# Optimization experiments

Hardware: AMD Instinct MI355X
Metric: run time of the kernel (lower is better)

Reference implementation:

```python
import jax, jax.numpy as jnp
import numpy as np

N = 50000          # nodes
E = 1_600_000      # edges
DIN = 128          # input feature dim
HID = 32           # hidden_dim per head
HEADS = 4          # conv1 heads
G = 64             # graphs in batch
SLOPE = 0.2        # LeakyReLU negative slope (PyG GATConv default)
EPS = 1e-16


def setup_inputs() -> dict:
    key = jax.random.key(0)
    ks = jax.random.split(key, 14)
    s = 0.05
    return {
        "x": jax.random.normal(ks[0], (N, DIN), jnp.float32),
        "edge_index": jax.random.randint(ks[1], (2, E), 0, N, dtype=jnp.int64),
        "batch": jnp.sort(jax.random.randint(ks[2], (N,), 0, G, dtype=jnp.int64)),
        # conv1: GATConv(DIN, HID, heads=4, concat=True)
        "W1": jax.random.normal(ks[3], (DIN, HEADS * HID), jnp.float32) * s,
        "a_src1": jax.random.normal(ks[4], (HEADS, HID), jnp.float32) * s,
        "a_dst1": jax.random.normal(ks[5], (HEADS, HID), jnp.float32) * s,
        "b1": jax.random.normal(ks[6], (HEADS * HID,), jnp.float32) * s,
        # conv2: GATConv(4*HID, HID, heads=1)
        "W2": jax.random.normal(ks[7], (HEADS * HID, HID), jnp.float32) * s,
        "a_src2": jax.random.normal(ks[8], (1, HID), jnp.float32) * s,
        "a_dst2": jax.random.normal(ks[9], (1, HID), jnp.float32) * s,
        "b2": jax.random.normal(ks[10], (HID,), jnp.float32) * s,
        # final Linear(HID, 2)
        "Wfc": jax.random.normal(ks[11], (HID, 2), jnp.float32) * s,
        "bfc": jax.random.normal(ks[12], (2,), jnp.float32) * s,
    }


def gat_conv(x, src, dst, W, a_src, a_dst, b, heads, d):
    """PyG-style GATConv (self-loops already appended to src/dst)."""
    n = x.shape[0]
    h = (x @ W).reshape(n, heads, d)                   # [N,H,D]
    alpha_src = jnp.einsum('nhd,hd->nh', h, a_src)     # [N,H]
    alpha_dst = jnp.einsum('nhd,hd->nh', h, a_dst)     # [N,H]
    e = alpha_src[src] + alpha_dst[dst]                # [Etot,H]
    e = jnp.where(e >= 0, e, SLOPE * e)                # LeakyReLU
    # segment softmax over destination nodes
    m = jax.ops.segment_max(e, dst, num_segments=n)    # [N,H]
    e = jnp.exp(e - m[dst])
    s = jax.ops.segment_sum(e, dst, num_segments=n)    # [N,H]
    alpha = e / (s[dst] + EPS)                         # [Etot,H]
    msg = h[src] * alpha[:, :, None]                   # [Etot,H,D]
    out = jax.ops.segment_sum(msg, dst, num_segments=n)  # [N,H,D]
    return out.reshape(n, heads * d) + b               # concat heads + bias


def reference(x, edge_index, batch, W1, a_src1, a_dst1, b1,
              W2, a_src2, a_dst2, b2, Wfc, bfc):
    n = x.shape[0]
    loops = jnp.arange(n, dtype=edge_index.dtype)
    src = jnp.concatenate([edge_index[0], loops])      # add self loops
    dst = jnp.concatenate([edge_index[1], loops])

    h = gat_conv(x, src, dst, W1, a_src1, a_dst1, b1, HEADS, HID)
    h = jax.nn.elu(h)
    h = gat_conv(h, src, dst, W2, a_src2, a_dst2, b2, 1, HID)
    h = jax.nn.elu(h)

    # global mean pool over graphs
    sums = jax.ops.segment_sum(h, batch, num_segments=G)            # [G,HID]
    cnt = jax.ops.segment_sum(jnp.ones((n, 1), h.dtype), batch, num_segments=G)
    pooled = sums / jnp.maximum(cnt, 1.0)

    logits = pooled @ Wfc + bfc                                      # [G,2]
    return jax.nn.log_softmax(logits, axis=1)
```

## Files before the change

### kernel.cpp

```cpp
#include <hip/hip_runtime.h>
#include <hip/hip_fp8.h>
#include <math.h>

#define DIN   128
#define HEADS 4
#define HID   32
#define C1    (HEADS*HID)
#define NG    64
#define SLOPE 0.2f
#define EPSF  1e-16f

#define NPB   256
#define CAPQ  10240
#define CHUNK 2048

__device__ __forceinline__ unsigned int f2bf(float f) {
    unsigned int u = __float_as_uint(f);
    return (u + 0x7FFFu + ((u >> 16) & 1u)) >> 16;
}
__device__ __forceinline__ float bf_lo(unsigned int u) { return __uint_as_float(u << 16); }
__device__ __forceinline__ float bf_hi(unsigned int u) { return __uint_as_float(u & 0xFFFF0000u); }

__device__ __forceinline__ unsigned int f2fp8(float f) {
    __hip_fp8_e4m3 t(f);
    return (unsigned int)t.__x;
}
template <int SEL>
__device__ __forceinline__ float fp8tof(unsigned int u) {
#if __has_builtin(__builtin_amdgcn_cvt_f32_fp8)
    return __builtin_amdgcn_cvt_f32_fp8(u, SEL);
#else
    __hip_fp8_e4m3 t; t.__x = (unsigned char)((u >> (8 * SEL)) & 0xFFu); return (float)t;
#endif
}

template <int NT>
__device__ __forceinline__ int blockScanExcl(int v, int* wsum) {
    int lane = threadIdx.x & 63, wid = threadIdx.x >> 6;
    int incl = v;
#pragma unroll
    for (int d = 1; d < 64; d <<= 1) {
        int t = __shfl_up(incl, d);
        if (lane >= d) incl += t;
    }
    if (lane == 63) wsum[wid] = incl;
    __syncthreads();
    if (threadIdx.x == 0) {
        int a = 0;
#pragma unroll
        for (int w = 0; w < NT / 64; w++) { int t = wsum[w]; wsum[w] = a; a += t; }
    }
    __syncthreads();
    return incl - v + wsum[wid];
}

__global__ void k_zero(int* gcursor, float* pooled, int nbuck) {
    int i = blockIdx.x * blockDim.x + threadIdx.x;
    if (i < nbuck) gcursor[i] = 0;
    if (i < NG * HID) pooled[i] = 0.0f;
}

__global__ __launch_bounds__(256) void k_binscatter(const int* __restrict__ srcs,
        const int* __restrict__ dsts, int* __restrict__ gcursor,
        unsigned int* __restrict__ stage, int E) {
    __shared__ unsigned int s_tmp[CHUNK];
    __shared__ unsigned int s_out[CHUNK];
    __shared__ int s_hist[256], s_off[256], s_base[256], s_cur[256], wsum[4];
    int tid = threadIdx.x;
    int e0 = blockIdx.x * CHUNK;
    int cnt = min(CHUNK, E - e0);
    s_hist[tid] = 0;
    __syncthreads();
    for (int i = tid; i < cnt; i += 256) {
        int sv = srcs[e0 + i];
        int dv = dsts[e0 + i];
        int b = dv >> 8;
        s_tmp[i] = ((unsigned)b << 24) | ((unsigned)(dv & (NPB - 1)) << 16) | (unsigned)sv;
        atomicAdd(&s_hist[b], 1);
    }
    __syncthreads();
    int myc = s_hist[tid];
    int excl = blockScanExcl<256>(myc, wsum);
    s_off[tid] = excl;
    s_base[tid] = myc ? atomicAdd(&gcursor[tid], myc) : 0;
    s_cur[tid] = 0;
    __syncthreads();
    for (int i = tid; i < cnt; i += 256) {
        unsigned int p = s_tmp[i];
        int b = p >> 24;
        int pos = s_off[b] + atomicAdd(&s_cur[b], 1);
        s_out[pos] = p;
    }
    __syncthreads();
    for (int i = tid; i < cnt; i += 256) {
        unsigned int p = s_out[i];
        int b = p >> 24;
        int rel = s_base[b] + (i - s_off[b]);
        if (rel < CAPQ) stage[(size_t)b * CAPQ + rel] = p & 0xFFFFFFu;
    }
}

__global__ void k_bucketscan(int* __restrict__ gcursor, int* __restrict__ ebase, int nbuck) {
    __shared__ int wsum[4];
    int tid = threadIdx.x;
    int c = (tid < nbuck) ? min(gcursor[tid], CAPQ) : 0;
    int excl = blockScanExcl<256>(c, wsum);
    if (tid < nbuck) { ebase[tid] = excl; gcursor[tid] = c; }
}

__global__ __launch_bounds__(512) void k_bucket_build(const unsigned int* __restrict__ stage,
        const int* __restrict__ gcursor, const int* __restrict__ ebase,
        int* __restrict__ rowstart, int* __restrict__ rowlen,
        int* __restrict__ esrc, int n) {
    __shared__ unsigned int s_e[CAPQ];
    __shared__ int s_cnt[256], s_offn[256], s_curn[256], wsum[8];
    int bx = blockIdx.x, tid = threadIdx.x;
    int b = bx >> 1, hf = bx & 1;
    int cnt = gcursor[b];
    int eb = ebase[b];
    int node0 = b << 8;
    for (int i = tid; i < cnt; i += 512) s_e[i] = stage[(size_t)b * CAPQ + i];
    if (tid < 256) { s_cnt[tid] = 0; s_curn[tid] = 0; }
    __syncthreads();
    for (int i = tid; i < cnt; i += 512) atomicAdd(&s_cnt[s_e[i] >> 16], 1);
    __syncthreads();
    int myc = (tid < 256) ? s_cnt[tid] : 0;
    int excl = blockScanExcl<512>(myc, wsum);
    if (tid < 256) s_offn[tid] = excl;
    __syncthreads();
    if (tid < 128) {
        int ld = (hf << 7) + tid;
        int node = node0 + ld;
        if (node < n) { rowstart[node] = eb + s_offn[ld]; rowlen[node] = s_cnt[ld]; }
    }
    for (int i = tid; i < cnt; i += 512) {
        unsigned int p = s_e[i];
        int ld = p >> 16;
        if ((ld >> 7) == hf) {
            int pos = s_offn[ld] + atomicAdd(&s_curn[ld], 1);
            esrc[eb + pos] = (int)(p & 0xFFFFu);
        }
    }
}

#define BM1 64
#define BK1 32
__global__ __launch_bounds__(256) void k_conv1(const float* __restrict__ x, const float* __restrict__ W1,
                        const float* __restrict__ a_src, const float* __restrict__ a_dst,
                        unsigned char* __restrict__ h1f8, float* __restrict__ as1,
                        float* __restrict__ ad1, int n) {
    __shared__ float xt[BK1][BM1 + 1];
    __shared__ float ws[BK1][C1];
    int tid = threadIdx.x;
    int m0 = blockIdx.x * BM1;
    int ty = tid >> 4;
    int tx = tid & 15;
    int r0 = ty * 4;
    int c0 = tx * 8;
    float acc[4][8];
#pragma unroll
    for (int i = 0; i < 4; i++)
#pragma unroll
        for (int j = 0; j < 8; j++) acc[i][j] = 0.0f;

    for (int kb = 0; kb < DIN; kb += BK1) {
        {
            int row = tid >> 3;
            int c4  = (tid & 7) * 4;
#pragma unroll
            for (int i = 0; i < 2; i++) {
                int rr = row + i * 32;
                int g = m0 + rr;
                float4 v = make_float4(0.f, 0.f, 0.f, 0.f);
                if (g < n) v = *reinterpret_cast<const float4*>(x + (size_t)g * DIN + kb + c4);
                xt[c4 + 0][rr] = v.x; xt[c4 + 1][rr] = v.y;
                xt[c4 + 2][rr] = v.z; xt[c4 + 3][rr] = v.w;
            }
            int c4w = (tid & 31) * 4;
            int k0  = tid >> 5;
#pragma unroll
            for (int i = 0; i < 4; i++) {
                int kk = k0 + i * 8;
                *reinterpret_cast<float4*>(&ws[kk][c4w]) =
                    *reinterpret_cast<const float4*>(W1 + (size_t)(kb + kk) * C1 + c4w);
            }
        }
        __syncthreads();
#pragma unroll
        for (int kk = 0; kk < BK1; kk++) {
            float a[4], bb[8];
            *reinterpret_cast<float4*>(a)      = *reinterpret_cast<float4*>(&xt[kk][r0]);
            *reinterpret_cast<float4*>(bb)     = *reinterpret_cast<float4*>(&ws[kk][c0]);
            *reinterpret_cast<float4*>(bb + 4) = *reinterpret_cast<float4*>(&ws[kk][c0 + 4]);
#pragma unroll
            for (int i = 0; i < 4; i++)
#pragma unroll
                for (int j = 0; j < 8; j++) acc[i][j] = fmaf(a[i], bb[j], acc[i][j]);
        }
        __syncthreads();
    }
    float asv[8], adv[8];
#pragma unroll
    for (int j = 0; j < 8; j++) { asv[j] = a_src[c0 + j]; adv[j] = a_dst[c0 + j]; }
#pragma unroll
    for (int i = 0; i < 4; i++) {
        int g = m0 + r0 + i;
        float ps = 0.0f, pd = 0.0f;
#pragma unroll
        for (int j = 0; j < 8; j++) {
            ps = fmaf(acc[i][j], asv[j], ps);
            pd = fmaf(acc[i][j], adv[j], pd);
        }
        if (g < n) {
            unsigned int w0 = 0, w1 = 0;
#pragma unroll
            for (int j = 0; j < 4; j++) w0 |= f2fp8(acc[i][j]) << (8 * j);
#pragma unroll
            for (int j = 0; j < 4; j++) w1 |= f2fp8(acc[i][4 + j]) << (8 * j);
            *reinterpret_cast<uint2*>(h1f8 + (size_t)g * C1 + c0) = make_uint2(w0, w1);
        }
        ps += __shfl_xor(ps, 1); ps += __shfl_xor(ps, 2);
        pd += __shfl_xor(pd, 1); pd += __shfl_xor(pd, 2);
        if ((tx & 3) == 0 && g < n) {
            as1[g * HEADS + (tx >> 2)] = ps;
            ad1[g * HEADS + (tx >> 2)] = pd;
        }
    }
}

#define BM2 128
#define BK2 32
__global__ __launch_bounds__(256) void k_conv2(const unsigned int* __restrict__ x2u,
                        const float* __restrict__ W2,
                        const float* __restrict__ a_src, const float* __restrict__ a_dst,
                        unsigned char* __restrict__ h2f8, float* __restrict__ as2,
                        float* __restrict__ ad2, int n) {
    __shared__ float xt[BK2][BM2 + 1];
    __shared__ float ws[BK2][HID];
    int tid = threadIdx.x;
    int m0 = blockIdx.x * BM2;
    int ty = tid >> 3;
    int tx = tid & 7;
    int r0 = ty * 4;
    int c0 = tx * 4;
    float acc[4][4];
#pragma unroll
    for (int i = 0; i < 4; i++)
#pragma unroll
        for (int j = 0; j < 4; j++) acc[i][j] = 0.0f;

    for (int kb = 0; kb < C1; kb += BK2) {
        {
            int row = tid >> 3;
            int c4  = (tid & 7) * 4;
#pragma unroll
            for (int i = 0; i < 4; i++) {
                int rr = row + i * 32;
                int g = m0 + rr;
                uint2 u = make_uint2(0u, 0u);
                if (g < n) u = *reinterpret_cast<const uint2*>(x2u + (size_t)g * 64 + ((kb + c4) >> 1));
                xt[c4 + 0][rr] = bf_lo(u.x); xt[c4 + 1][rr] = bf_hi(u.x);
                xt[c4 + 2][rr] = bf_lo(u.y); xt[c4 + 3][rr] = bf_hi(u.y);
            }
            int kk = tid >> 3;
            int c4w = (tid & 7) * 4;
            *reinterpret_cast<float4*>(&ws[kk][c4w]) =
                *reinterpret_cast<const float4*>(W2 + (size_t)(kb + kk) * HID + c4w);
        }
        __syncthreads();
#pragma unroll
        for (int kk = 0; kk < BK2; kk++) {
            float a[4], bb[4];
            *reinterpret_cast<float4*>(a)  = *reinterpret_cast<float4*>(&xt[kk][r0]);
            *reinterpret_cast<float4*>(bb) = *reinterpret_cast<float4*>(&ws[kk][c0]);
#pragma unroll
            for (int i = 0; i < 4; i++)
#pragma unroll
                for (int j = 0; j < 4; j++) acc[i][j] = fmaf(a[i], bb[j], acc[i][j]);
        }
        __syncthreads();
    }
    float asv[4], adv[4];
#pragma unroll
    for (int j = 0; j < 4; j++) { asv[j] = a_src[c0 + j]; adv[j] = a_dst[c0 + j]; }
#pragma unroll
    for (int i = 0; i < 4; i++) {
        int g = m0 + r0 + i;
        float ps = 0.0f, pd = 0.0f;
#pragma unroll
        for (int j = 0; j < 4; j++) {
            ps = fmaf(acc[i][j], asv[j], ps);
            pd = fmaf(acc[i][j], adv[j], pd);
        }
        if (g < n) {
            unsigned int w = 0;
#pragma unroll
            for (int j = 0; j < 4; j++) w |= f2fp8(acc[i][j]) << (8 * j);
            *reinterpret_cast<unsigned int*>(h2f8 + (size_t)g * HID + c0) = w;
        }
        ps += __shfl_xor(ps, 1); ps += __shfl_xor(ps, 2); ps += __shfl_xor(ps, 4);
        pd += __shfl_xor(pd, 1); pd += __shfl_xor(pd, 2); pd += __shfl_xor(pd, 4);
        if (tx == 0 && g < n) { as2[g] = ps; ad2[g] = pd; }
    }
}

__global__ __launch_bounds__(256) void k_gat1(const int* __restrict__ rowstart, const int* __restrict__ rowlen,
                       const int* __restrict__ esrc,
                       const float* __restrict__ as1, const float* __restrict__ ad1,
                       const unsigned char* __restrict__ h1f8, const float* __restrict__ b1,
                       unsigned int* __restrict__ x2u, int n) {
    __shared__ float alds[4][64 * HEADS];
    __shared__ int   slds[4][64];
    const unsigned short* h1h = (const unsigned short*)h1f8;
    int wid = threadIdx.x >> 6;
    int lane = threadIdx.x & 63;
    int nid = blockIdx.x * 4 + wid;
    bool active = nid < n;
    int start = 0, deg = 0, cnt = 1;
    if (active) { start = rowstart[nid]; deg = rowlen[nid]; cnt = deg + 1; }
    bool fast = active && (cnt <= 64);

    float adv[HEADS] = {0.f, 0.f, 0.f, 0.f};
    if (active) {
#pragma unroll
        for (int h = 0; h < HEADS; h++) adv[h] = ad1[nid * HEADS + h];
    }

    if (fast) {
        int s = nid;
        if (lane < deg) s = esrc[start + lane];
        bool act = lane < cnt;
        float4 asv = make_float4(0.f, 0.f, 0.f, 0.f);
        if (act) asv = *reinterpret_cast<const float4*>(as1 + (size_t)s * HEADS);
        float v[HEADS];
        v[0] = asv.x + adv[0]; v[1] = asv.y + adv[1];
        v[2] = asv.z + adv[2]; v[3] = asv.w + adv[3];
        float p[HEADS], sum[HEADS];
#pragma unroll
        for (int h = 0; h < HEADS; h++) {
            v[h] = (v[h] >= 0.0f) ? v[h] : SLOPE * v[h];
            p[h] = act ? __expf(v[h]) : 0.0f;
            sum[h] = p[h];
#pragma unroll
            for (int off = 32; off; off >>= 1) sum[h] += __shfl_xor(sum[h], off);
            p[h] *= 1.0f / (sum[h] + EPSF);
        }
        slds[wid][lane] = s;
        float4 pv; pv.x = p[0]; pv.y = p[1]; pv.z = p[2]; pv.w = p[3];
        *reinterpret_cast<float4*>(&alds[wid][lane * 4]) = pv;
    }
    __syncthreads();
    if (!active) return;

    int j = lane * 2;
    int hme = lane >> 4;
    if (fast) {
        float accx = 0.0f, accy = 0.0f;
        int k = 0;
        for (; k + 3 < cnt; k += 4) {
            int s0 = slds[wid][k],     s1 = slds[wid][k + 1];
            int s2 = slds[wid][k + 2], s3 = slds[wid][k + 3];
            float a0 = alds[wid][k * 4 + hme],       a1 = alds[wid][(k + 1) * 4 + hme];
            float a2 = alds[wid][(k + 2) * 4 + hme], a3 = alds[wid][(k + 3) * 4 + hme];
            unsigned int u0 = h1h[(size_t)s0 * 64 + lane];
            unsigned int u1 = h1h[(size_t)s1 * 64 + lane];
            unsigned int u2 = h1h[(size_t)s2 * 64 + lane];
            unsigned int u3 = h1h[(size_t)s3 * 64 + lane];
            accx = fmaf(fp8tof<0>(u0), a0, accx); accy = fmaf(fp8tof<1>(u0), a0, accy);
            accx = fmaf(fp8tof<0>(u1), a1, accx); accy = fmaf(fp8tof<1>(u1), a1, accy);
            accx = fmaf(fp8tof<0>(u2), a2, accx); accy = fmaf(fp8tof<1>(u2), a2, accy);
            accx = fmaf(fp8tof<0>(u3), a3, accx); accy = fmaf(fp8tof<1>(u3), a3, accy);
        }
        for (; k < cnt; k++) {
            int s0 = slds[wid][k];
            float a0 = alds[wid][k * 4 + hme];
            unsigned int u0 = h1h[(size_t)s0 * 64 + lane];
            accx = fmaf(fp8tof<0>(u0), a0, accx); accy = fmaf(fp8tof<1>(u0), a0, accy);
        }
        float o0 = accx + b1[j], o1 = accy + b1[j + 1];
        o0 = (o0 > 0.0f) ? o0 : expm1f(o0);
        o1 = (o1 > 0.0f) ? o1 : expm1f(o1);
        x2u[(size_t)nid * 64 + lane] = f2bf(o0) | (f2bf(o1) << 16);
    } else {
        float m[HEADS] = {-INFINITY, -INFINITY, -INFINITY, -INFINITY};
        for (int k = lane; k <= deg; k += 64) {
            int s = (k < deg) ? esrc[start + k] : nid;
#pragma unroll
            for (int h = 0; h < HEADS; h++) {
                float v = as1[s * HEADS + h] + adv[h];
                v = (v >= 0.0f) ? v : SLOPE * v;
                m[h] = fmaxf(m[h], v);
            }
        }
#pragma unroll
        for (int h = 0; h < HEADS; h++)
#pragma unroll
            for (int off = 32; off; off >>= 1) m[h] = fmaxf(m[h], __shfl_xor(m[h], off));
        float sum[HEADS] = {0.f, 0.f, 0.f, 0.f};
        for (int k = lane; k <= deg; k += 64) {
            int s = (k < deg) ? esrc[start + k] : nid;
#pragma unroll
            for (int h = 0; h < HEADS; h++) {
                float v = as1[s * HEADS + h] + adv[h];
                v = (v >= 0.0f) ? v : SLOPE * v;
                sum[h] += __expf(v - m[h]);
            }
        }
#pragma unroll
        for (int h = 0; h < HEADS; h++) {
#pragma unroll
            for (int off = 32; off; off >>= 1) sum[h] += __shfl_xor(sum[h], off);
            sum[h] = 1.0f / (sum[h] + EPSF);
        }
        float adme = adv[hme], mme = m[hme], invme = sum[hme];
        float accx = 0.0f, accy = 0.0f;
        for (int k = 0; k <= deg; k++) {
            int s = (k < deg) ? esrc[start + k] : nid;
            float v = as1[s * HEADS + hme] + adme;
            v = (v >= 0.0f) ? v : SLOPE * v;
            float alpha = __expf(v - mme) * invme;
            unsigned int u0 = h1h[(size_t)s * 64 + lane];
            accx = fmaf(fp8tof<0>(u0), alpha, accx);
            accy = fmaf(fp8tof<1>(u0), alpha, accy);
        }
        float o0 = accx + b1[j], o1 = accy + b1[j + 1];
        o0 = (o0 > 0.0f) ? o0 : expm1f(o0);
        o1 = (o1 > 0.0f) ? o1 : expm1f(o1);
        x2u[(size_t)nid * 64 + lane] = f2bf(o0) | (f2bf(o1) << 16);
    }
}

__global__ __launch_bounds__(256) void k_gat2(const int* __restrict__ rowstart, const int* __restrict__ rowlen,
                       const int* __restrict__ esrc,
                       const float* __restrict__ as2, const float* __restrict__ ad2,
                       const unsigned char* __restrict__ h2f8, const float* __restrict__ b2,
                       float* __restrict__ x3, int n) {
    __shared__ float alds[4][64];
    __shared__ int   slds[4][64];
    const unsigned short* h2h = (const unsigned short*)h2f8;
    int wid = threadIdx.x >> 6;
    int lane = threadIdx.x & 63;
    int nid = blockIdx.x * 4 + wid;
    bool active = nid < n;
    int start = 0, deg = 0, cnt = 1;
    float adv = 0.0f;
    if (active) { start = rowstart[nid]; deg = rowlen[nid]; cnt = deg + 1; adv = ad2[nid]; }
    bool fast = active && (cnt <= 64);

    if (fast) {
        int s = nid;
        if (lane < deg) s = esrc[start + lane];
        bool act = lane < cnt;
        float v = as2[s] + adv;
        v = (v >= 0.0f) ? v : SLOPE * v;
        float p = act ? __expf(v) : 0.0f;
        float sum = p;
#pragma unroll
        for (int off = 32; off; off >>= 1) sum += __shfl_xor(sum, off);
        p *= 1.0f / (sum + EPSF);
        slds[wid][lane] = s;
        alds[wid][lane] = p;
    }
    __syncthreads();
    if (!active) return;

    if (fast) {
        int q = lane >> 4, l = lane & 15;
        float acc0 = 0.0f, acc1 = 0.0f;
#pragma unroll 2
        for (int k = q; k < cnt; k += 4) {
            int s = slds[wid][k];
            float a = alds[wid][k];
            unsigned int u = h2h[(size_t)s * 16 + l];
            acc0 = fmaf(fp8tof<0>(u), a, acc0);
            acc1 = fmaf(fp8tof<1>(u), a, acc1);
        }
        acc0 += __shfl_xor(acc0, 16); acc0 += __shfl_xor(acc0, 32);
        acc1 += __shfl_xor(acc1, 16); acc1 += __shfl_xor(acc1, 32);
        if (q == 0) {
            int c0 = l * 2;
            float o0 = acc0 + b2[c0], o1 = acc1 + b2[c0 + 1];
            o0 = (o0 > 0.0f) ? o0 : expm1f(o0);
            o1 = (o1 > 0.0f) ? o1 : expm1f(o1);
            float2 r; r.x = o0; r.y = o1;
            *reinterpret_cast<float2*>(x3 + (size_t)nid * HID + c0) = r;
        }
    } else {
        int c = lane & 31;
        int half = lane >> 5;
        float m = -INFINITY;
        for (int k = lane; k <= deg; k += 64) {
            int s = (k < deg) ? esrc[start + k] : nid;
            float v = as2[s] + adv;
            v = (v >= 0.0f) ? v : SLOPE * v;
            m = fmaxf(m, v);
        }
#pragma unroll
        for (int off = 32; off; off >>= 1) m = fmaxf(m, __shfl_xor(m, off));
        float sum = 0.0f;
        for (int k = lane; k <= deg; k += 64) {
            int s = (k < deg) ? esrc[start + k] : nid;
            float v = as2[s] + adv;
            v = (v >= 0.0f) ? v : SLOPE * v;
            sum += __expf(v - m);
        }
#pragma unroll
        for (int off = 32; off; off >>= 1) sum += __shfl_xor(sum, off);
        float inv = 1.0f / (sum + EPSF);
        float acc = 0.0f;
        for (int k = half; k <= deg; k += 2) {
            int s = (k < deg) ? esrc[start + k] : nid;
            float v = as2[s] + adv;
            v = (v >= 0.0f) ? v : SLOPE * v;
            float alpha = __expf(v - m) * inv;
            unsigned int u = h2h[(size_t)s * 16 + (c >> 1)];
            float hv = (c & 1) ? fp8tof<1>(u) : fp8tof<0>(u);
            acc = fmaf(hv, alpha, acc);
        }
        acc += __shfl_xor(acc, 32);
        if (half == 0) {
            float o = acc + b2[c];
            o = (o > 0.0f) ? o : expm1f(o);
            x3[(size_t)nid * HID + c] = o;
        }
    }
}

__device__ __forceinline__ int lower_bound_g(const int* batch, int n, int g) {
    int lo = 0, hi = n;
    while (lo < hi) {
        int mid = (lo + hi) >> 1;
        if (batch[mid] < g) lo = mid + 1; else hi = mid;
    }
    return lo;
}

__global__ void k_pool(const float* __restrict__ x3, const int* __restrict__ batch,
                       float* __restrict__ pooled, int n) {
    int g = blockIdx.x >> 2, part = blockIdx.x & 3;
    int start = lower_bound_g(batch, n, g);
    int end   = lower_bound_g(batch, n, g + 1);
    int c = threadIdx.x & 31;
    int row = threadIdx.x >> 5;
    float acc = 0.0f;
    for (int i = start + part * 8 + row; i < end; i += 32)
        acc += x3[(size_t)i * HID + c];
    __shared__ float sacc[8][HID];
    sacc[row][c] = acc;
    __syncthreads();
    if (row == 0) {
        float a = 0.0f;
#pragma unroll
        for (int p = 0; p < 8; p++) a += sacc[p][c];
        atomicAdd(&pooled[g * HID + c], a);
    }
}

__global__ void k_head(const float* __restrict__ pooled, const int* __restrict__ batch, int n,
                       const float* __restrict__ Wfc, const float* __restrict__ bfc,
                       float* __restrict__ out, int g_count) {
    int g = blockIdx.x * blockDim.x + threadIdx.x;
    if (g >= g_count) return;
    int start = lower_bound_g(batch, n, g);
    int end   = lower_bound_g(batch, n, g + 1);
    float inv = 1.0f / fmaxf((float)(end - start), 1.0f);
    float l0 = bfc[0], l1 = bfc[1];
#pragma unroll
    for (int d = 0; d < HID; d++) {
        float p = pooled[g * HID + d] * inv;
        l0 = fmaf(p, Wfc[d * 2 + 0], l0);
        l1 = fmaf(p, Wfc[d * 2 + 1], l1);
    }
    float mx = fmaxf(l0, l1);
    float lse = mx + logf(expf(l0 - mx) + expf(l1 - mx));
    out[g * 2 + 0] = l0 - lse;
    out[g * 2 + 1] = l1 - lse;
}

extern "C" void kernel_launch(void* const* d_in, const int* in_sizes, int n_in,
                              void* d_out, int out_size, void* d_ws, size_t ws_size,
                              hipStream_t stream) {
    const float* x      = (const float*)d_in[0];
    const int*   ei     = (const int*)d_in[1];
    const int*   batch  = (const int*)d_in[2];
    const float* W1     = (const float*)d_in[3];
    const float* a_src1 = (const float*)d_in[4];
    const float* a_dst1 = (const float*)d_in[5];
    const float* b1     = (const float*)d_in[6];
    const float* W2     = (const float*)d_in[7];
    const float* a_src2 = (const float*)d_in[8];
    const float* a_dst2 = (const float*)d_in[9];
    const float* b2     = (const float*)d_in[10];
    const float* Wfc    = (const float*)d_in[11];
    const float* bfc    = (const float*)d_in[12];
    float* out = (float*)d_out;

    const int n = in_sizes[2];
    const int E = in_sizes[1] / 2;
    const int nbuck = (n + NPB - 1) / NPB;

    const int* srcs = ei;
    const int* dsts = ei + E;

    unsigned char* h1f8 = (unsigned char*)d_ws;
    unsigned int*  x2u  = (unsigned int*)(h1f8 + (size_t)n * C1);
    unsigned char* h2f8 = (unsigned char*)(x2u + (size_t)n * 64);
    float* x3     = (float*)(h2f8 + (size_t)n * HID);
    float* as1    = x3  + (size_t)n * HID;
    float* ad1    = as1 + (size_t)n * HEADS;
    float* as2    = ad1 + (size_t)n * HEADS;
    float* ad2    = as2 + (size_t)n;
    float* pooled = ad2 + (size_t)n;
    int* rowstart = (int*)(pooled + NG * HID);
    int* rowlen   = rowstart + n;
    int* esrc     = rowlen + n;
    int* gcursor  = esrc + E;
    int* ebase    = gcursor + 256;
    unsigned int* stage = (unsigned int*)(ebase + 256);

    k_zero<<<8, 256, 0, stream>>>(gcursor, pooled, nbuck);
    k_binscatter<<<(E + CHUNK - 1) / CHUNK, 256, 0, stream>>>(srcs, dsts, gcursor, stage, E);
    k_bucketscan<<<1, 256, 0, stream>>>(gcursor, ebase, nbuck);
    k_bucket_build<<<nbuck * 2, 512, 0, stream>>>(stage, gcursor, ebase, rowstart, rowlen, esrc, n);

    k_conv1<<<(n + BM1 - 1) / BM1, 256, 0, stream>>>(x, W1, a_src1, a_dst1, h1f8, as1, ad1, n);

    k_gat1<<<(n + 3) / 4, 256, 0, stream>>>(rowstart, rowlen, esrc, as1, ad1, h1f8, b1, x2u, n);

    k_conv2<<<(n + BM2 - 1) / BM2, 256, 0, stream>>>(x2u, W2, a_src2, a_dst2, h2f8, as2, ad2, n);

    k_gat2<<<(n + 3) / 4, 256, 0, stream>>>(rowstart, rowlen, esrc, as2, ad2, h2f8, b2, x3, n);

    k_pool<<<NG * 4, 256, 0, stream>>>(x3, batch, pooled, n);

    k_head<<<1, 64, 0, stream>>>(pooled, batch, n, Wfc, bfc, out, NG);
}
```

Measured before the change: 275.2 us.

## Drop bucket-scan and pooled-zero launches, widen conv1 tile, vectorize gat1 gather

```diff
diff --git a/kernel.cpp b/kernel.cpp
--- a/kernel.cpp
+++ b/kernel.cpp
@@ -33,6 +33,15 @@
     __hip_fp8_e4m3 t; t.__x = (unsigned char)((u >> (8 * SEL)) & 0xFFu); return (float)t;
 #endif
 }
+typedef float f32x2 __attribute__((ext_vector_type(2)));
+template <int WORD>
+__device__ __forceinline__ f32x2 fp8pk(unsigned int u) {
+#if __has_builtin(__builtin_amdgcn_cvt_pk_f32_fp8)
+    return __builtin_amdgcn_cvt_pk_f32_fp8((int)u, WORD);
+#else
+    f32x2 r; r[0] = fp8tof<2 * WORD>(u); r[1] = fp8tof<2 * WORD + 1>(u); return r;
+#endif
+}
 
 template <int NT>
 __device__ __forceinline__ int blockScanExcl(int v, int* wsum) {
@@ -54,10 +63,9 @@
     return incl - v + wsum[wid];
 }
 
-__global__ void k_zero(int* gcursor, float* pooled, int nbuck) {
-    int i = blockIdx.x * blockDim.x + threadIdx.x;
+__global__ void k_zero(int* gcursor, int nbuck) {
+    int i = threadIdx.x;
     if (i < nbuck) gcursor[i] = 0;
-    if (i < NG * HID) pooled[i] = 0.0f;
 }
 
 __global__ __launch_bounds__(256) void k_binscatter(const int* __restrict__ srcs,
@@ -100,30 +108,28 @@
     }
 }
 
-__global__ void k_bucketscan(int* __restrict__ gcursor, int* __restrict__ ebase, int nbuck) {
-    __shared__ int wsum[4];
-    int tid = threadIdx.x;
-    int c = (tid < nbuck) ? min(gcursor[tid], CAPQ) : 0;
-    int excl = blockScanExcl<256>(c, wsum);
-    if (tid < nbuck) { ebase[tid] = excl; gcursor[tid] = c; }
-}
-
 __global__ __launch_bounds__(512) void k_bucket_build(const unsigned int* __restrict__ stage,
-        const int* __restrict__ gcursor, const int* __restrict__ ebase,
+        const int* __restrict__ gcursor,
         int* __restrict__ rowstart, int* __restrict__ rowlen,
         int* __restrict__ esrc, int n) {
     __shared__ unsigned int s_e[CAPQ];
     __shared__ int s_cnt[256], s_offn[256], s_curn[256], wsum[8];
+    __shared__ int s_eb;
     int bx = blockIdx.x, tid = threadIdx.x;
     int b = bx >> 1, hf = bx & 1;
-    int cnt = gcursor[b];
-    int eb = ebase[b];
+    int cnt = min(gcursor[b], CAPQ);
     int node0 = b << 8;
-    for (int i = tid; i < cnt; i += 512) s_e[i] = stage[(size_t)b * CAPQ + i];
+    if (tid == 0) s_eb = 0;
     if (tid < 256) { s_cnt[tid] = 0; s_curn[tid] = 0; }
     __syncthreads();
-    for (int i = tid; i < cnt; i += 512) atomicAdd(&s_cnt[s_e[i] >> 16], 1);
-    __syncthreads();
+    if (tid < b) atomicAdd(&s_eb, min(gcursor[tid], CAPQ));
+    for (int i = tid; i < cnt; i += 512) {
+        unsigned int p = stage[(size_t)b * CAPQ + i];
+        s_e[i] = p;
+        atomicAdd(&s_cnt[p >> 16], 1);
+    }
+    __syncthreads();
+    int eb = s_eb;
     int myc = (tid < 256) ? s_cnt[tid] : 0;
     int excl = blockScanExcl<512>(myc, wsum);
     if (tid < 256) s_offn[tid] = excl;
@@ -143,7 +149,7 @@
     }
 }
 
-#define BM1 64
+#define BM1 128
 #define BK1 32
 __global__ __launch_bounds__(256) void k_conv1(const float* __restrict__ x, const float* __restrict__ W1,
                         const float* __restrict__ a_src, const float* __restrict__ a_dst,
@@ -155,11 +161,11 @@
     int m0 = blockIdx.x * BM1;
     int ty = tid >> 4;
     int tx = tid & 15;
-    int r0 = ty * 4;
+    int r0 = ty * 8;
     int c0 = tx * 8;
-    float acc[4][8];
-#pragma unroll
-    for (int i = 0; i < 4; i++)
+    float acc[8][8];
+#pragma unroll
+    for (int i = 0; i < 8; i++)
 #pragma unroll
         for (int j = 0; j < 8; j++) acc[i][j] = 0.0f;
 
@@ -168,7 +174,7 @@
             int row = tid >> 3;
             int c4  = (tid & 7) * 4;
 #pragma unroll
-            for (int i = 0; i < 2; i++) {
+            for (int i = 0; i < 4; i++) {
                 int rr = row + i * 32;
                 int g = m0 + rr;
                 float4 v = make_float4(0.f, 0.f, 0.f, 0.f);
@@ -188,12 +194,13 @@
         __syncthreads();
 #pragma unroll
         for (int kk = 0; kk < BK1; kk++) {
-            float a[4], bb[8];
+            float a[8], bb[8];
             *reinterpret_cast<float4*>(a)      = *reinterpret_cast<float4*>(&xt[kk][r0]);
+            *reinterpret_cast<float4*>(a + 4)  = *reinterpret_cast<float4*>(&xt[kk][r0 + 4]);
             *reinterpret_cast<float4*>(bb)     = *reinterpret_cast<float4*>(&ws[kk][c0]);
             *reinterpret_cast<float4*>(bb + 4) = *reinterpret_cast<float4*>(&ws[kk][c0 + 4]);
 #pragma unroll
-            for (int i = 0; i < 4; i++)
+            for (int i = 0; i < 8; i++)
 #pragma unroll
                 for (int j = 0; j < 8; j++) acc[i][j] = fmaf(a[i], bb[j], acc[i][j]);
         }
@@ -203,7 +210,7 @@
 #pragma unroll
     for (int j = 0; j < 8; j++) { asv[j] = a_src[c0 + j]; adv[j] = a_dst[c0 + j]; }
 #pragma unroll
-    for (int i = 0; i < 4; i++) {
+    for (int i = 0; i < 8; i++) {
         int g = m0 + r0 + i;
         float ps = 0.0f, pd = 0.0f;
 #pragma unroll
@@ -311,6 +318,7 @@
                        unsigned int* __restrict__ x2u, int n) {
     __shared__ float alds[4][64 * HEADS];
     __shared__ int   slds[4][64];
+    const uint2* h1u2 = (const uint2*)h1f8;
     const unsigned short* h1h = (const unsigned short*)h1f8;
     int wid = threadIdx.x >> 6;
     int lane = threadIdx.x & 63;
@@ -352,36 +360,46 @@
     __syncthreads();
     if (!active) return;
 
-    int j = lane * 2;
-    int hme = lane >> 4;
     if (fast) {
-        float accx = 0.0f, accy = 0.0f;
-        int k = 0;
-        for (; k + 3 < cnt; k += 4) {
-            int s0 = slds[wid][k],     s1 = slds[wid][k + 1];
-            int s2 = slds[wid][k + 2], s3 = slds[wid][k + 3];
-            float a0 = alds[wid][k * 4 + hme],       a1 = alds[wid][(k + 1) * 4 + hme];
-            float a2 = alds[wid][(k + 2) * 4 + hme], a3 = alds[wid][(k + 3) * 4 + hme];
-            unsigned int u0 = h1h[(size_t)s0 * 64 + lane];
-            unsigned int u1 = h1h[(size_t)s1 * 64 + lane];
-            unsigned int u2 = h1h[(size_t)s2 * 64 + lane];
-            unsigned int u3 = h1h[(size_t)s3 * 64 + lane];
-            accx = fmaf(fp8tof<0>(u0), a0, accx); accy = fmaf(fp8tof<1>(u0), a0, accy);
-            accx = fmaf(fp8tof<0>(u1), a1, accx); accy = fmaf(fp8tof<1>(u1), a1, accy);
-            accx = fmaf(fp8tof<0>(u2), a2, accx); accy = fmaf(fp8tof<1>(u2), a2, accy);
-            accx = fmaf(fp8tof<0>(u3), a3, accx); accy = fmaf(fp8tof<1>(u3), a3, accy);
-        }
-        for (; k < cnt; k++) {
-            int s0 = slds[wid][k];
-            float a0 = alds[wid][k * 4 + hme];
-            unsigned int u0 = h1h[(size_t)s0 * 64 + lane];
-            accx = fmaf(fp8tof<0>(u0), a0, accx); accy = fmaf(fp8tof<1>(u0), a0, accy);
-        }
-        float o0 = accx + b1[j], o1 = accy + b1[j + 1];
-        o0 = (o0 > 0.0f) ? o0 : expm1f(o0);
-        o1 = (o1 > 0.0f) ? o1 : expm1f(o1);
-        x2u[(size_t)nid * 64 + lane] = f2bf(o0) | (f2bf(o1) << 16);
+        int q = lane >> 4, l = lane & 15;
+        int hq = l >> 2;
+        float acc[8];
+#pragma unroll
+        for (int i = 0; i < 8; i++) acc[i] = 0.0f;
+#pragma unroll 2
+        for (int k = q; k < cnt; k += 4) {
+            int s = slds[wid][k];
+            float a = alds[wid][k * 4 + hq];
+            uint2 u = h1u2[(size_t)s * 16 + l];
+            f32x2 f0 = fp8pk<0>(u.x), f1 = fp8pk<1>(u.x);
+            f32x2 f2 = fp8pk<0>(u.y), f3 = fp8pk<1>(u.y);
+            acc[0] = fmaf(f0[0], a, acc[0]); acc[1] = fmaf(f0[1], a, acc[1]);
+            acc[2] = fmaf(f1[0], a, acc[2]); acc[3] = fmaf(f1[1], a, acc[3]);
+            acc[4] = fmaf(f2[0], a, acc[4]); acc[5] = fmaf(f2[1], a, acc[5]);
+            acc[6] = fmaf(f3[0], a, acc[6]); acc[7] = fmaf(f3[1], a, acc[7]);
+        }
+#pragma unroll
+        for (int i = 0; i < 8; i++) {
+            acc[i] += __shfl_xor(acc[i], 16);
+            acc[i] += __shfl_xor(acc[i], 32);
+        }
+        if (q == 0) {
+            int j0 = l * 8;
+            unsigned int w[4];
+#pragma unroll
+            for (int i = 0; i < 4; i++) {
+                float o0 = acc[2 * i] + b1[j0 + 2 * i];
+                float o1 = acc[2 * i + 1] + b1[j0 + 2 * i + 1];
+                o0 = (o0 > 0.0f) ? o0 : expm1f(o0);
+                o1 = (o1 > 0.0f) ? o1 : expm1f(o1);
+                w[i] = f2bf(o0) | (f2bf(o1) << 16);
+            }
+            *reinterpret_cast<uint4*>(x2u + (size_t)nid * 64 + l * 4) =
+                make_uint4(w[0], w[1], w[2], w[3]);
+        }
     } else {
+        int j = lane * 2;
+        int hme = lane >> 4;
         float m[HEADS] = {-INFINITY, -INFINITY, -INFINITY, -INFINITY};
         for (int k = lane; k <= deg; k += 64) {
             int s = (k < deg) ? esrc[start + k] : nid;
@@ -472,8 +490,9 @@
             int s = slds[wid][k];
             float a = alds[wid][k];
             unsigned int u = h2h[(size_t)s * 16 + l];
-            acc0 = fmaf(fp8tof<0>(u), a, acc0);
-            acc1 = fmaf(fp8tof<1>(u), a, acc1);
+            f32x2 f = fp8pk<0>(u);
+            acc0 = fmaf(f[0], a, acc0);
+            acc1 = fmaf(f[1], a, acc1);
         }
         acc0 += __shfl_xor(acc0, 16); acc0 += __shfl_xor(acc0, 32);
         acc1 += __shfl_xor(acc1, 16); acc1 += __shfl_xor(acc1, 32);
@@ -535,39 +554,37 @@
     return lo;
 }
 
-__global__ void k_pool(const float* __restrict__ x3, const int* __restrict__ batch,
+__global__ __launch_bounds__(512) void k_pool(const float* __restrict__ x3,
+                       const int* __restrict__ batch,
                        float* __restrict__ pooled, int n) {
-    int g = blockIdx.x >> 2, part = blockIdx.x & 3;
+    int g = blockIdx.x;
     int start = lower_bound_g(batch, n, g);
     int end   = lower_bound_g(batch, n, g + 1);
     int c = threadIdx.x & 31;
     int row = threadIdx.x >> 5;
     float acc = 0.0f;
-    for (int i = start + part * 8 + row; i < end; i += 32)
+    for (int i = start + row; i < end; i += 16)
         acc += x3[(size_t)i * HID + c];
-    __shared__ float sacc[8][HID];
+    __shared__ float sacc[16][HID];
     sacc[row][c] = acc;
     __syncthreads();
     if (row == 0) {
         float a = 0.0f;
 #pragma unroll
-        for (int p = 0; p < 8; p++) a += sacc[p][c];
-        atomicAdd(&pooled[g * HID + c], a);
-    }
-}
-
-__global__ void k_head(const float* __restrict__ pooled, const int* __restrict__ batch, int n,
-                       const float* __restrict__ Wfc, const float* __restrict__ bfc,
-                       float* __restrict__ out, int g_count) {
+        for (int p = 0; p < 16; p++) a += sacc[p][c];
+        float cntf = (float)(end - start);
+        pooled[g * HID + c] = a / fmaxf(cntf, 1.0f);
+    }
+}
+
+__global__ void k_head(const float* __restrict__ pooled, const float* __restrict__ Wfc,
+                       const float* __restrict__ bfc, float* __restrict__ out, int g_count) {
     int g = blockIdx.x * blockDim.x + threadIdx.x;
     if (g >= g_count) return;
-    int start = lower_bound_g(batch, n, g);
-    int end   = lower_bound_g(batch, n, g + 1);
-    float inv = 1.0f / fmaxf((float)(end - start), 1.0f);
     float l0 = bfc[0], l1 = bfc[1];
 #pragma unroll
     for (int d = 0; d < HID; d++) {
-        float p = pooled[g * HID + d] * inv;
+        float p = pooled[g * HID + d];
         l0 = fmaf(p, Wfc[d * 2 + 0], l0);
         l1 = fmaf(p, Wfc[d * 2 + 1], l1);
     }
@@ -615,13 +632,11 @@
     int* rowlen   = rowstart + n;
     int* esrc     = rowlen + n;
     int* gcursor  = esrc + E;
-    int* ebase    = gcursor + 256;
-    unsigned int* stage = (unsigned int*)(ebase + 256);
-
-    k_zero<<<8, 256, 0, stream>>>(gcursor, pooled, nbuck);
+    unsigned int* stage = (unsigned int*)(gcursor + 256);
+
+    k_zero<<<1, 256, 0, stream>>>(gcursor, nbuck);
     k_binscatter<<<(E + CHUNK - 1) / CHUNK, 256, 0, stream>>>(srcs, dsts, gcursor, stage, E);
-    k_bucketscan<<<1, 256, 0, stream>>>(gcursor, ebase, nbuck);
-    k_bucket_build<<<nbuck * 2, 512, 0, stream>>>(stage, gcursor, ebase, rowstart, rowlen, esrc, n);
+    k_bucket_build<<<nbuck * 2, 512, 0, stream>>>(stage, gcursor, rowstart, rowlen, esrc, n);
 
     k_conv1<<<(n + BM1 - 1) / BM1, 256, 0, stream>>>(x, W1, a_src1, a_dst1, h1f8, as1, ad1, n);
 
@@ -631,7 +646,7 @@
 
     k_gat2<<<(n + 3) / 4, 256, 0, stream>>>(rowstart, rowlen, esrc, as2, ad2, h2f8, b2, x3, n);
 
-    k_pool<<<NG * 4, 256, 0, stream>>>(x3, batch, pooled, n);
-
-    k_head<<<1, 64, 0, stream>>>(pooled, batch, n, Wfc, bfc, out, NG);
-}
+    k_pool<<<NG, 512, 0, stream>>>(x3, batch, pooled, n);
+
+    k_head<<<1, 64, 0, stream>>>(pooled, Wfc, bfc, out, NG);
+}
```

Result: slower. 294.3 us (+7.0%).
